# Optimization experiments

Measured on AMD Instinct MI355X. Metric: run time of the kernel, lower is better.

The kernel has to match this reference:

```python
import jax, jax.numpy as jnp
import numpy as np

H = 1024   # hidden_size == memory_size
NH = 4     # num_attention_heads
HD = H // NH
M = 8192   # total memory items
B, S = 4, 2048
EPS = 1e-5


def _ln(x, g, b):
    mu = jnp.mean(x, -1, keepdims=True)
    var = jnp.mean((x - mu) ** 2, -1, keepdims=True)
    return (x - mu) / jnp.sqrt(var + EPS) * g + b


def setup_inputs() -> dict:
    key = jax.random.key(0)
    ks = jax.random.split(key, 16)
    s = 0.02
    return {
        "query_hidden": jax.random.normal(ks[0], (B, S, H), jnp.float32),
        "mem_keys": jax.random.normal(ks[1], (M, H), jnp.float32),
        "importance": jax.random.uniform(ks[2], (M,), jnp.float32),
        "recency": jax.random.uniform(ks[3], (M,), jnp.float32),
        "access_count": jax.random.uniform(ks[4], (M,), jnp.float32),
        "Wq": s * jax.random.normal(ks[5], (H, H), jnp.float32),
        "bq": jnp.zeros((H,), jnp.float32),
        "in_w": s * jax.random.normal(ks[6], (3 * H, H), jnp.float32),
        "in_b": jnp.zeros((3 * H,), jnp.float32),
        "out_w": s * jax.random.normal(ks[7], (H, H), jnp.float32),
        "out_b": jnp.zeros((H,), jnp.float32),
        "gate_w": s * jax.random.normal(ks[8], (H, 2 * H), jnp.float32),
        "gate_b": jnp.zeros((H,), jnp.float32),
        "int_w1": s * jax.random.normal(ks[9], (2 * H, 2 * H), jnp.float32),
        "int_b1": jnp.zeros((2 * H,), jnp.float32),
        "int_ln_g": jnp.ones((2 * H,), jnp.float32),
        "int_ln_b": jnp.zeros((2 * H,), jnp.float32),
        "int_w2": s * jax.random.normal(ks[10], (H, 2 * H), jnp.float32),
        "int_b2": jnp.zeros((H,), jnp.float32),
        "ln1_g": jnp.ones((H,), jnp.float32),
        "ln1_b": jnp.zeros((H,), jnp.float32),
        "ln2_g": jnp.ones((H,), jnp.float32),
        "ln2_b": jnp.zeros((H,), jnp.float32),
        "sel_params": jnp.ones((3,), jnp.float32) / 3.0,
        "top_k": 2048,
    }


def reference(query_hidden, mem_keys, importance, recency, access_count,
              Wq, bq, in_w, in_b, out_w, out_b, gate_w, gate_b,
              int_w1, int_b1, int_ln_g, int_ln_b, int_w2, int_b2,
              ln1_g, ln1_b, ln2_g, ln2_b, sel_params, top_k):
    b, s, _ = query_hidden.shape
    # HTPS selection: softmax-weighted mix of importance / recency / frequency
    w = jax.nn.softmax(sel_params)
    freq = access_count / jnp.max(access_count)
    sel = w[0] * importance + w[1] * recency + w[2] * freq
    _, idx = jax.lax.top_k(sel, top_k)
    mem = mem_keys[idx]                      # [K, H]
    mem_n = _ln(mem, ln1_g, ln1_b)           # layer_norm1 on memory

    q = query_hidden @ Wq.T + bq             # query_proj  [B,S,H]
    wq, wk, wv = in_w[:H], in_w[H:2 * H], in_w[2 * H:]
    bqi, bki, bvi = in_b[:H], in_b[H:2 * H], in_b[2 * H:]
    # Batched MHA: the per-position loop is equivalent to all S queries at once
    Q = (q @ wq.T + bqi).reshape(b, s, NH, HD)
    K = (mem_n @ wk.T + bki).reshape(top_k, NH, HD)   # shared across batch
    V = (mem_n @ wv.T + bvi).reshape(top_k, NH, HD)
    scores = jnp.einsum('bshd,khd->bhsk', Q, K) / jnp.sqrt(jnp.float32(HD))
    attn = jax.nn.softmax(scores, axis=-1)
    ctx = jnp.einsum('bhsk,khd->bshd', attn, V).reshape(b, s, H)
    attn_out = ctx @ out_w.T + out_b

    cat = jnp.concatenate([query_hidden, attn_out], axis=-1)   # [B,S,2H]
    gate = jax.nn.sigmoid(cat @ gate_w.T + gate_b)
    h1 = _ln(cat @ int_w1.T + int_b1, int_ln_g, int_ln_b)
    integ = jax.nn.gelu(h1, approximate=False) @ int_w2.T + int_b2
    return _ln(query_hidden + gate * integ, ln2_g, ln2_b)
```

## Files before the change

### kernel.cpp

```cpp
#include <hip/hip_runtime.h>

#define HDIM 1024
#define MMEM 8192
#define TOPK 2048
#define NROWS 8192
#define LNEPS 1e-5f

typedef unsigned short ushort_t;
typedef __bf16 bf16x8 __attribute__((ext_vector_type(8)));
typedef float f32x4 __attribute__((ext_vector_type(4)));
typedef __attribute__((address_space(1))) const void GVoid;
typedef __attribute__((address_space(3))) void LVoid;

__device__ __forceinline__ ushort_t f2bf(float f) {
    union { float f; unsigned u; } c; c.f = f;
    unsigned r = c.u + 0x7fffu + ((c.u >> 16) & 1u);
    return (ushort_t)(r >> 16);
}
__device__ __forceinline__ float bf2f(ushort_t u) {
    union { unsigned u; float f; } c; c.u = ((unsigned)u) << 16; return c.f;
}
__device__ __forceinline__ float blk_red(float v, int op, float* red) {
    #pragma unroll
    for (int o = 32; o; o >>= 1) {
        float u = __shfl_down(v, o);
        v = op ? fmaxf(v, u) : v + u;
    }
    if ((threadIdx.x & 63) == 0) red[threadIdx.x >> 6] = v;
    __syncthreads();
    float r = op ? fmaxf(fmaxf(red[0], red[1]), fmaxf(red[2], red[3]))
                 : (red[0] + red[1]) + (red[2] + red[3]);
    __syncthreads();
    return r;
}

__global__ __launch_bounds__(256) void sel_prep(const float* __restrict__ sp,
        const float* __restrict__ imp, const float* __restrict__ rec,
        const float* __restrict__ ac, float* __restrict__ sel) {
    __shared__ float red[4];
    float p0 = sp[0], p1 = sp[1], p2 = sp[2];
    float mx = fmaxf(p0, fmaxf(p1, p2));
    float e0 = expf(p0 - mx), e1 = expf(p1 - mx), e2 = expf(p2 - mx);
    float inv = 1.f / (e0 + e1 + e2);
    float w0 = e0 * inv, w1 = e1 * inv, w2 = e2 * inv;
    float m = -1e30f;
    for (int i = threadIdx.x; i < MMEM; i += 256) m = fmaxf(m, ac[i]);
    m = blk_red(m, 1, red);
    float rinv = 1.f / m;
    for (int i = threadIdx.x; i < MMEM; i += 256)
        sel[i] = w0 * imp[i] + w1 * rec[i] + w2 * (ac[i] * rinv);
}

__global__ __launch_bounds__(256) void topk_rank(const float* __restrict__ sel,
                                                 int* __restrict__ idx) {
    __shared__ float s[MMEM];
    __shared__ int pc[256];
    for (int t = threadIdx.x; t < MMEM / 4; t += 256)
        reinterpret_cast<float4*>(s)[t] = reinterpret_cast<const float4*>(sel)[t];
    __syncthreads();
    const int li = threadIdx.x & 31;
    const int jc = threadIdx.x >> 5;
    const int i  = blockIdx.x * 32 + li;
    const float si = s[i];
    int cnt = 0;
    const float4* sv = reinterpret_cast<const float4*>(s) + jc * 256;
    #pragma unroll 4
    for (int t = 0; t < 256; ++t) {
        float4 v = sv[t];
        int j0 = jc * 1024 + t * 4;
        cnt += (v.x > si) || (v.x == si && (j0 + 0) < i);
        cnt += (v.y > si) || (v.y == si && (j0 + 1) < i);
        cnt += (v.z > si) || (v.z == si && (j0 + 2) < i);
        cnt += (v.w > si) || (v.w == si && (j0 + 3) < i);
    }
    pc[threadIdx.x] = cnt;
    __syncthreads();
    if (threadIdx.x < 32) {
        int r = 0;
        #pragma unroll
        for (int c = 0; c < 8; ++c) r += pc[c * 32 + threadIdx.x];
        if (r < TOPK) idx[r] = blockIdx.x * 32 + threadIdx.x;
    }
}

__global__ __launch_bounds__(256) void gather_ln(const float* __restrict__ mem_keys,
        const int* __restrict__ idx, const float* __restrict__ g,
        const float* __restrict__ b, ushort_t* __restrict__ out) {
    __shared__ float red[4];
    int src = idx[blockIdx.x] & (MMEM - 1);
    const float* x = mem_keys + (size_t)src * HDIM;
    float4 v = reinterpret_cast<const float4*>(x)[threadIdx.x];
    float s = v.x + v.y + v.z + v.w;
    float ss = v.x*v.x + v.y*v.y + v.z*v.z + v.w*v.w;
    s  = blk_red(s, 0, red);
    ss = blk_red(ss, 0, red);
    float mu = s * (1.f / HDIM);
    float var = ss * (1.f / HDIM) - mu * mu;
    float rstd = rsqrtf(var + LNEPS);
    int c = threadIdx.x * 4;
    ushort4 o;
    o.x = f2bf((v.x - mu) * rstd * g[c+0] + b[c+0]);
    o.y = f2bf((v.y - mu) * rstd * g[c+1] + b[c+1]);
    o.z = f2bf((v.z - mu) * rstd * g[c+2] + b[c+2]);
    o.w = f2bf((v.w - mu) * rstd * g[c+3] + b[c+3]);
    *reinterpret_cast<ushort4*>(out + (size_t)blockIdx.x * HDIM + c) = o;
}

__global__ __launch_bounds__(256) void cvt_all(const float* __restrict__ in_w,
        const float* __restrict__ out_w, const float* __restrict__ gate_w,
        const float* __restrict__ int_w1, const float* __restrict__ int_w2,
        ushort_t* __restrict__ inw_bf, ushort_t* __restrict__ outw_bf,
        ushort_t* __restrict__ gw3, ushort_t* __restrict__ intw2_bf) {
    const int b = blockIdx.x;
    const float* src; ushort_t* dst; int rel;
    if      (b < 3072)  { src = in_w;   dst = inw_bf;        rel = b; }
    else if (b < 4096)  { src = out_w;  dst = outw_bf;       rel = b - 3072; }
    else if (b < 6144)  { src = gate_w; dst = gw3;           rel = b - 4096; }
    else if (b < 10240) { src = int_w1; dst = gw3 + 2097152; rel = b - 6144; }
    else                { src = int_w2; dst = intw2_bf;      rel = b - 10240; }
    size_t i = ((size_t)rel * 256 + threadIdx.x) * 4;
    float4 v = *reinterpret_cast<const float4*>(src + i);
    ushort4 o = { f2bf(v.x), f2bf(v.y), f2bf(v.z), f2bf(v.w) };
    *reinterpret_cast<ushort4*>(dst + i) = o;
}

__global__ __launch_bounds__(256) void cvt_t_bf16(const float* __restrict__ in,
                                                  ushort_t* __restrict__ out) {
    __shared__ ushort_t t[64][65];
    const int bx = blockIdx.x * 64, by = blockIdx.y * 64;
    const int r = threadIdx.x >> 4, c4 = (threadIdx.x & 15) << 2;
    #pragma unroll
    for (int rr = 0; rr < 64; rr += 16) {
        float4 v = *reinterpret_cast<const float4*>(in + (size_t)(by + r + rr) * 1024 + bx + c4);
        t[r + rr][c4 + 0] = f2bf(v.x);
        t[r + rr][c4 + 1] = f2bf(v.y);
        t[r + rr][c4 + 2] = f2bf(v.z);
        t[r + rr][c4 + 3] = f2bf(v.w);
    }
    __syncthreads();
    #pragma unroll
    for (int rr = 0; rr < 64; rr += 16) {
        const int i = r + rr;
        ushort4 o = { t[c4 + 0][i], t[c4 + 1][i], t[c4 + 2][i], t[c4 + 3][i] };
        *reinterpret_cast<ushort4*>(out + (size_t)(bx + i) * 1024 + by + c4) = o;
    }
}

__global__ __launch_bounds__(256) void bias_fold(const float* __restrict__ wq,
        const float* __restrict__ bq, const float* __restrict__ bqi,
        float* __restrict__ beff) {
    __shared__ float red[4];
    const float4 wv = reinterpret_cast<const float4*>(wq + (size_t)blockIdx.x * 1024)[threadIdx.x];
    const float4 bv = reinterpret_cast<const float4*>(bq)[threadIdx.x];
    float s = wv.x*bv.x + wv.y*bv.y + wv.z*bv.z + wv.w*bv.w;
    s = blk_red(s, 0, red);
    if (threadIdx.x == 0) beff[blockIdx.x] = s + bqi[blockIdx.x];
}

__global__ __launch_bounds__(256) void cvt_x_cat(const float* __restrict__ x,
                                                 ushort_t* __restrict__ cat) {
    size_t i = ((size_t)blockIdx.x * 256 + threadIdx.x) * 4;
    size_t row = i >> 10, col = i & 1023;
    float4 v = *reinterpret_cast<const float4*>(x + i);
    ushort4 o = { f2bf(v.x), f2bf(v.y), f2bf(v.z), f2bf(v.w) };
    *reinterpret_cast<ushort4*>(cat + row * 2048 + col) = o;
}

__global__ __launch_bounds__(256) void softmax_rows(ushort_t* __restrict__ sc) {
    const int row = blockIdx.x * 4 + (threadIdx.x >> 6);
    const int l = threadIdx.x & 63;
    uint4* p = reinterpret_cast<uint4*>(sc + (size_t)row * 2048 + l * 32);
    uint4 u[4];
    #pragma unroll
    for (int i = 0; i < 4; ++i) u[i] = p[i];
    float v[32];
    #pragma unroll
    for (int i = 0; i < 4; ++i) {
        unsigned* w = reinterpret_cast<unsigned*>(&u[i]);
        #pragma unroll
        for (int k = 0; k < 4; ++k) {
            union { unsigned u; float f; } lo, hi;
            lo.u = w[k] << 16; hi.u = w[k] & 0xffff0000u;
            v[i*8 + k*2]     = lo.f;
            v[i*8 + k*2 + 1] = hi.f;
        }
    }
    float mx = v[0];
    #pragma unroll
    for (int j = 1; j < 32; ++j) mx = fmaxf(mx, v[j]);
    #pragma unroll
    for (int o = 1; o < 64; o <<= 1) mx = fmaxf(mx, __shfl_xor(mx, o));
    float s = 0.f;
    #pragma unroll
    for (int j = 0; j < 32; ++j) { v[j] = expf(v[j] - mx); s += v[j]; }
    #pragma unroll
    for (int o = 1; o < 64; o <<= 1) s += __shfl_xor(s, o);
    float inv = 1.f / s;
    #pragma unroll
    for (int i = 0; i < 4; ++i) {
        unsigned* w = reinterpret_cast<unsigned*>(&u[i]);
        #pragma unroll
        for (int k = 0; k < 4; ++k) {
            unsigned lo = f2bf(v[i*8 + k*2] * inv);
            unsigned hi = f2bf(v[i*8 + k*2 + 1] * inv);
            w[k] = lo | (hi << 16);
        }
    }
    #pragma unroll
    for (int i = 0; i < 4; ++i) p[i] = u[i];
}

__global__ __launch_bounds__(256) void ln_gelu(ushort_t* h1,
        const float* __restrict__ g, const float* __restrict__ b) {
    __shared__ float red[4];
    ushort_t* p = h1 + (size_t)blockIdx.x * 2048 + threadIdx.x * 8;
    ushort4 a = reinterpret_cast<const ushort4*>(p)[0];
    ushort4 c = reinterpret_cast<const ushort4*>(p)[1];
    float v[8] = { bf2f(a.x), bf2f(a.y), bf2f(a.z), bf2f(a.w),
                   bf2f(c.x), bf2f(c.y), bf2f(c.z), bf2f(c.w) };
    float s = 0.f, ss = 0.f;
    #pragma unroll
    for (int j = 0; j < 8; ++j) { s += v[j]; ss += v[j]*v[j]; }
    s  = blk_red(s, 0, red);
    ss = blk_red(ss, 0, red);
    float mu = s * (1.f / 2048.f);
    float var = ss * (1.f / 2048.f) - mu * mu;
    float rstd = rsqrtf(var + LNEPS);
    int c0 = threadIdx.x * 8;
    ushort_t o[8];
    #pragma unroll
    for (int j = 0; j < 8; ++j) {
        float xn = (v[j] - mu) * rstd * g[c0 + j] + b[c0 + j];
        float ge = 0.5f * xn * (1.f + erff(xn * 0.70710678118654752f));
        o[j] = f2bf(ge);
    }
    ushort4 o1 = { o[0], o[1], o[2], o[3] };
    ushort4 o2 = { o[4], o[5], o[6], o[7] };
    reinterpret_cast<ushort4*>(p)[0] = o1;
    reinterpret_cast<ushort4*>(p)[1] = o2;
}

__global__ __launch_bounds__(256) void final_ln(const float* __restrict__ x,
        const ushort_t* __restrict__ gate, const ushort_t* __restrict__ integ,
        const float* __restrict__ g, const float* __restrict__ b,
        float* __restrict__ out) {
    __shared__ float red[4];
    size_t base = (size_t)blockIdx.x * HDIM + threadIdx.x * 4;
    float4 xv = *reinterpret_cast<const float4*>(x + base);
    ushort4 gv = *reinterpret_cast<const ushort4*>(gate + base);
    ushort4 iv = *reinterpret_cast<const ushort4*>(integ + base);
    float v[4] = { xv.x + bf2f(gv.x)*bf2f(iv.x), xv.y + bf2f(gv.y)*bf2f(iv.y),
                   xv.z + bf2f(gv.z)*bf2f(iv.z), xv.w + bf2f(gv.w)*bf2f(iv.w) };
    float s = v[0]+v[1]+v[2]+v[3];
    float ss = v[0]*v[0]+v[1]*v[1]+v[2]*v[2]+v[3]*v[3];
    s  = blk_red(s, 0, red);
    ss = blk_red(ss, 0, red);
    float mu = s * (1.f / HDIM);
    float var = ss * (1.f / HDIM) - mu * mu;
    float rstd = rsqrtf(var + LNEPS);
    int c = threadIdx.x * 4;
    float4 o;
    o.x = (v[0] - mu) * rstd * g[c+0] + b[c+0];
    o.y = (v[1] - mu) * rstd * g[c+1] + b[c+1];
    o.z = (v[2] - mu) * rstd * g[c+2] + b[c+2];
    o.w = (v[3] - mu) * rstd * g[c+3] + b[c+3];
    *reinterpret_cast<float4*>(out + base) = o;
}

template<int EPI, int BIAS>
__global__ __launch_bounds__(256, 2)
void gemm_bt(const ushort_t* __restrict__ A, const ushort_t* __restrict__ B,
             const float* __restrict__ bias, void* __restrict__ Cv,
             void* __restrict__ Cv2, const float* __restrict__ bias2,
             int K, int lda, int ldb, int ldc,
             long long sA1, long long sA2, long long sAz,
             long long sB1, long long sB2, long long sBz,
             long long sC1, long long sC2, long long sCz,
             int z2n, int zbase, float scale)
{
    __shared__ __align__(16) ushort_t As[8192];
    __shared__ __align__(16) ushort_t Bs[8192];
    const int zz = blockIdx.z;
    const int zg = zz + zbase;
    const int z1 = zg / z2n, z2 = zg - z1 * z2n;
    A += (size_t)(z1 * sA1 + z2 * sA2 + zz * sAz);
    B += (size_t)(z1 * sB1 + z2 * sB2 + zz * sBz);
    const size_t cOff = (size_t)(z1 * sC1 + z2 * sC2 + zz * sCz);

    const int nwg = gridDim.x * gridDim.y;
    const int wg  = blockIdx.y * gridDim.x + blockIdx.x;
    const int q8  = nwg >> 3, r8 = nwg & 7;
    const int xcd = wg & 7, lo = wg >> 3;
    const int wgid = (xcd < r8 ? xcd * (q8 + 1) : r8 * (q8 + 1) + (xcd - r8) * q8) + lo;
    const int m0 = (wgid / gridDim.x) * 128, n0 = (wgid % gridDim.x) * 128;

    const int tid = threadIdx.x;
    const int w = tid >> 6, l = tid & 63;
    const int wm = w >> 1, wn = w & 1;

    f32x4 acc[4][4] = {};
    const int srow = l >> 3;
    const int scol = ((l & 7) ^ srow) << 3;

    for (int k0 = 0; k0 < K; k0 += 64) {
        #pragma unroll
        for (int i = 0; i < 4; ++i) {
            const int c = i * 4 + w;
            const int row = c * 8 + srow;
            const ushort_t* ga = A + (size_t)(m0 + row) * lda + (k0 + scol);
            const ushort_t* gb = B + (size_t)(n0 + row) * ldb + (k0 + scol);
            __builtin_amdgcn_global_load_lds((GVoid*)ga, (LVoid*)(As + c * 512), 16, 0, 0);
            __builtin_amdgcn_global_load_lds((GVoid*)gb, (LVoid*)(Bs + c * 512), 16, 0, 0);
        }
        __syncthreads();
        #pragma unroll
        for (int kk = 0; kk < 2; ++kk) {
            bf16x8 af[4], bfv[4];
            #pragma unroll
            for (int m = 0; m < 4; ++m) {
                const int row = wm * 64 + m * 16 + (l & 15);
                const int cb = ((kk * 64) + ((l >> 4) * 16)) ^ ((row & 7) << 4);
                af[m] = *reinterpret_cast<const bf16x8*>(
                    reinterpret_cast<const char*>(As) + row * 128 + cb);
            }
            #pragma unroll
            for (int n = 0; n < 4; ++n) {
                const int row = wn * 64 + n * 16 + (l & 15);
                const int cb = ((kk * 64) + ((l >> 4) * 16)) ^ ((row & 7) << 4);
                bfv[n] = *reinterpret_cast<const bf16x8*>(
                    reinterpret_cast<const char*>(Bs) + row * 128 + cb);
            }
            #pragma unroll
            for (int m = 0; m < 4; ++m)
                #pragma unroll
                for (int n = 0; n < 4; ++n)
                    acc[m][n] = __builtin_amdgcn_mfma_f32_16x16x32_bf16(
                        af[m], bfv[n], acc[m][n], 0, 0, 0);
        }
        __syncthreads();
    }

    #pragma unroll
    for (int m = 0; m < 4; ++m) {
        const int grow = m0 + wm * 64 + m * 16 + ((l >> 4) << 2);
        #pragma unroll
        for (int n = 0; n < 4; ++n) {
            const int gcol = n0 + wn * 64 + n * 16 + (l & 15);
            float bc = (BIAS == 1) ? bias[gcol] : 0.f;
            #pragma unroll
            for (int j = 0; j < 4; ++j) {
                if (EPI == 3) {
                    float v = acc[m][n][j];
                    if (gcol < 1024) {
                        v += bias[gcol];
                        v = 1.f / (1.f + expf(-v));
                        ((ushort_t*)Cv)[(size_t)(grow + j) * ldc + gcol] = f2bf(v);
                    } else {
                        v += bias2[gcol - 1024];
                        ((ushort_t*)Cv2)[(size_t)(grow + j) * 2048 + (gcol - 1024)] = f2bf(v);
                    }
                } else {
                    float v = acc[m][n][j] * scale;
                    if (BIAS == 1) v += bc;
                    if (BIAS == 2) v += bias[grow + j];
                    if (EPI == 2) v = 1.f / (1.f + expf(-v));
                    const size_t off = cOff + (size_t)(grow + j) * ldc + gcol;
                    if (EPI == 1) ((ushort_t*)Cv)[off] = f2bf(v);
                    else          ((float*)Cv)[off]    = v;
                }
            }
        }
    }
}

extern "C" void kernel_launch(void* const* d_in, const int* in_sizes, int n_in,
                              void* d_out, int out_size, void* d_ws, size_t ws_size,
                              hipStream_t stream) {
    const float* x          = (const float*)d_in[0];
    const float* mem_keys   = (const float*)d_in[1];
    const float* importance = (const float*)d_in[2];
    const float* recency    = (const float*)d_in[3];
    const float* access_cnt = (const float*)d_in[4];
    const float* Wq         = (const float*)d_in[5];
    const float* bq         = (const float*)d_in[6];
    const float* in_w       = (const float*)d_in[7];
    const float* in_b       = (const float*)d_in[8];
    const float* out_w      = (const float*)d_in[9];
    const float* out_b      = (const float*)d_in[10];
    const float* gate_w     = (const float*)d_in[11];
    const float* gate_b     = (const float*)d_in[12];
    const float* int_w1     = (const float*)d_in[13];
    const float* int_b1     = (const float*)d_in[14];
    const float* int_ln_g   = (const float*)d_in[15];
    const float* int_ln_b   = (const float*)d_in[16];
    const float* int_w2     = (const float*)d_in[17];
    const float* int_b2     = (const float*)d_in[18];
    const float* ln1_g      = (const float*)d_in[19];
    const float* ln1_b      = (const float*)d_in[20];
    const float* ln2_g      = (const float*)d_in[21];
    const float* ln2_b      = (const float*)d_in[22];
    const float* sel_params = (const float*)d_in[23];

    char* ws = (char*)d_ws;
    size_t off = 0;
    auto alloc = [&](size_t bytes) -> char* {
        char* p = ws + off;
        off = (off + bytes + 255) & ~(size_t)255;
        return p;
    };

    float*    sel      = (float*)alloc(MMEM * 4);
    int*      idx      = (int*)alloc(TOPK * 4);
    float*    beff     = (float*)alloc(1024 * 4);
    ushort_t* wqT_bf   = (ushort_t*)alloc((size_t)1048576 * 2);
    ushort_t* weff_bf  = (ushort_t*)alloc((size_t)1048576 * 2);
    ushort_t* inw_bf   = (ushort_t*)alloc((size_t)3145728 * 2);
    ushort_t* outw_bf  = (ushort_t*)alloc((size_t)1048576 * 2);
    ushort_t* gw3      = (ushort_t*)alloc((size_t)6291456 * 2);
    ushort_t* intw2_bf = (ushort_t*)alloc((size_t)2097152 * 2);
    ushort_t* mem_n    = (ushort_t*)alloc((size_t)TOPK * HDIM * 2);
    ushort_t* Kbuf     = (ushort_t*)alloc((size_t)TOPK * HDIM * 2);
    ushort_t* Vt       = (ushort_t*)alloc((size_t)HDIM * TOPK * 2);
    ushort_t* cat      = (ushort_t*)alloc((size_t)NROWS * 2048 * 2);
    ushort_t* qQ       = (ushort_t*)alloc((size_t)NROWS * 2048 * 2);
    ushort_t* Qbuf     = qQ + (size_t)NROWS * HDIM;
    ushort_t* h1       = qQ;
    ushort_t* ctx      = (ushort_t*)alloc((size_t)NROWS * HDIM * 2);
    ushort_t* integ    = ctx;

    int NC = 16;
    while (NC > 1 && off + (size_t)NC * 8388608 > ws_size) NC >>= 1;
    ushort_t* scores = (ushort_t*)alloc((size_t)NC * 8388608);
    ushort_t* gatev  = scores;

    cvt_t_bf16<<<dim3(16,16), 256, 0, stream>>>(Wq, wqT_bf);
    cvt_all<<<12288, 256, 0, stream>>>(in_w, out_w, gate_w, int_w1, int_w2,
                                       inw_bf, outw_bf, gw3, intw2_bf);
    cvt_x_cat<<<8192, 256, 0, stream>>>(x, cat);
    bias_fold<<<1024, 256, 0, stream>>>(in_w, bq, in_b, beff);

    gemm_bt<1,0><<<dim3(8,8,1), 256, 0, stream>>>(inw_bf, wqT_bf, nullptr, weff_bf,
        nullptr, nullptr, 1024, 1024, 1024, 1024, 0,0,0, 0,0,0, 0,0,0, 1, 0, 1.f);

    sel_prep<<<1, 256, 0, stream>>>(sel_params, importance, recency, access_cnt, sel);
    topk_rank<<<MMEM/32, 256, 0, stream>>>(sel, idx);
    gather_ln<<<TOPK, 256, 0, stream>>>(mem_keys, idx, ln1_g, ln1_b, mem_n);

    gemm_bt<1,1><<<dim3(8,64,1), 256, 0, stream>>>(cat, weff_bf, beff, Qbuf,
        nullptr, nullptr, 1024, 2048, 1024, 1024, 0,0,0, 0,0,0, 0,0,0, 1, 0, 1.f);
    gemm_bt<1,1><<<dim3(8,16,1), 256, 0, stream>>>(mem_n, inw_bf + 1048576, in_b + 1024,
        Kbuf, nullptr, nullptr, 1024, 1024, 1024, 1024, 0,0,0, 0,0,0, 0,0,0, 1, 0, 1.f);
    gemm_bt<1,2><<<dim3(16,8,1), 256, 0, stream>>>(inw_bf + 2097152, mem_n, in_b + 2048,
        Vt, nullptr, nullptr, 1024, 1024, 1024, 2048, 0,0,0, 0,0,0, 0,0,0, 1, 0, 1.f);

    for (int c0 = 0; c0 < 16; c0 += NC) {
        gemm_bt<1,0><<<dim3(16,16,NC), 256, 0, stream>>>(Qbuf, Kbuf, nullptr, scores,
            nullptr, nullptr, 256, 1024, 1024, 2048,
            2097152, 256, 0,  0, 256, 0,  0, 0, 4194304, 4, c0, 0.0625f);
        softmax_rows<<<NC * 512, 256, 0, stream>>>(scores);
        gemm_bt<1,0><<<dim3(2,16,NC), 256, 0, stream>>>(scores, Vt, nullptr, ctx,
            nullptr, nullptr, 2048, 2048, 2048, 1024,
            0, 0, 4194304,  0, 524288, 0,  2097152, 256, 0, 4, c0, 1.f);
    }

    gemm_bt<1,1><<<dim3(8,64,1), 256, 0, stream>>>(ctx, outw_bf, out_b,
        (void*)(cat + 1024), nullptr, nullptr, 1024, 1024, 1024, 2048,
        0,0,0, 0,0,0, 0,0,0, 1, 0, 1.f);

    gemm_bt<3,0><<<dim3(24,64,1), 256, 0, stream>>>(cat, gw3, gate_b, gatev,
        h1, int_b1, 2048, 2048, 2048, 1024, 0,0,0, 0,0,0, 0,0,0, 1, 0, 1.f);

    ln_gelu<<<NROWS, 256, 0, stream>>>(h1, int_ln_g, int_ln_b);
    gemm_bt<1,1><<<dim3(8,64,1), 256, 0, stream>>>(h1, intw2_bf, int_b2, integ,
        nullptr, nullptr, 2048, 2048, 2048, 1024, 0,0,0, 0,0,0, 0,0,0, 1, 0, 1.f);
    final_ln<<<NROWS, 256, 0, stream>>>(x, gatev, integ, ln2_g, ln2_b, (float*)d_out);
}
```

Measured before the change: 584.1 us.

## Fold out_proj into gate/int_w1 weights and split-K over x and ctx

Removes the separate out_proj GEMM by precomputing folded weights (the attn_out half of gate_w/int_w1 multiplied by out_w) and folded biases. The gate/int GEMM then reads x and ctx directly through a two-source split-K path instead of a materialized concat buffer, which saves an 8192x1024x1024 GEMM and the cat writes. The cost is a small weight-fold GEMM, an extra transpose-convert of out_w, and bias-fold kernels per call. It also swaps expf for __expf in the softmax and sigmoid epilogues, which slightly changes precision.

```diff
diff --git a/kernel.cpp b/kernel.cpp
--- a/kernel.cpp
+++ b/kernel.cpp
@@ -106,18 +106,25 @@
     *reinterpret_cast<ushort4*>(out + (size_t)blockIdx.x * HDIM + c) = o;
 }
 
+__global__ __launch_bounds__(256) void cvt_bf16(const float* __restrict__ in,
+                                                ushort_t* __restrict__ out) {
+    size_t i = ((size_t)blockIdx.x * 256 + threadIdx.x) * 4;
+    float4 v = *reinterpret_cast<const float4*>(in + i);
+    ushort4 o = { f2bf(v.x), f2bf(v.y), f2bf(v.z), f2bf(v.w) };
+    *reinterpret_cast<ushort4*>(out + i) = o;
+}
+
 __global__ __launch_bounds__(256) void cvt_all(const float* __restrict__ in_w,
-        const float* __restrict__ out_w, const float* __restrict__ gate_w,
-        const float* __restrict__ int_w1, const float* __restrict__ int_w2,
-        ushort_t* __restrict__ inw_bf, ushort_t* __restrict__ outw_bf,
-        ushort_t* __restrict__ gw3, ushort_t* __restrict__ intw2_bf) {
+        const float* __restrict__ gate_w, const float* __restrict__ int_w1,
+        const float* __restrict__ int_w2,
+        ushort_t* __restrict__ inw_bf, ushort_t* __restrict__ gw3,
+        ushort_t* __restrict__ intw2_bf) {
     const int b = blockIdx.x;
     const float* src; ushort_t* dst; int rel;
-    if      (b < 3072)  { src = in_w;   dst = inw_bf;        rel = b; }
-    else if (b < 4096)  { src = out_w;  dst = outw_bf;       rel = b - 3072; }
-    else if (b < 6144)  { src = gate_w; dst = gw3;           rel = b - 4096; }
-    else if (b < 10240) { src = int_w1; dst = gw3 + 2097152; rel = b - 6144; }
-    else                { src = int_w2; dst = intw2_bf;      rel = b - 10240; }
+    if      (b < 3072) { src = in_w;   dst = inw_bf;        rel = b; }
+    else if (b < 5120) { src = gate_w; dst = gw3;           rel = b - 3072; }
+    else if (b < 9216) { src = int_w1; dst = gw3 + 2097152; rel = b - 5120; }
+    else               { src = int_w2; dst = intw2_bf;      rel = b - 9216; }
     size_t i = ((size_t)rel * 256 + threadIdx.x) * 4;
     float4 v = *reinterpret_cast<const float4*>(src + i);
     ushort4 o = { f2bf(v.x), f2bf(v.y), f2bf(v.z), f2bf(v.w) };
@@ -157,13 +164,20 @@
     if (threadIdx.x == 0) beff[blockIdx.x] = s + bqi[blockIdx.x];
 }
 
-__global__ __launch_bounds__(256) void cvt_x_cat(const float* __restrict__ x,
-                                                 ushort_t* __restrict__ cat) {
-    size_t i = ((size_t)blockIdx.x * 256 + threadIdx.x) * 4;
-    size_t row = i >> 10, col = i & 1023;
-    float4 v = *reinterpret_cast<const float4*>(x + i);
-    ushort4 o = { f2bf(v.x), f2bf(v.y), f2bf(v.z), f2bf(v.w) };
-    *reinterpret_cast<ushort4*>(cat + row * 2048 + col) = o;
+__global__ __launch_bounds__(256) void bias_fold3(const float* __restrict__ gate_w,
+        const float* __restrict__ int_w1, const float* __restrict__ gate_b,
+        const float* __restrict__ int_b1, const float* __restrict__ out_b,
+        float* __restrict__ beff3) {
+    __shared__ float red[4];
+    const int j = blockIdx.x;
+    const float* wrow = (j < 1024 ? gate_w + (size_t)j * 2048
+                                  : int_w1 + (size_t)(j - 1024) * 2048) + 1024;
+    const float4 wv = reinterpret_cast<const float4*>(wrow)[threadIdx.x];
+    const float4 bv = reinterpret_cast<const float4*>(out_b)[threadIdx.x];
+    float s = wv.x*bv.x + wv.y*bv.y + wv.z*bv.z + wv.w*bv.w;
+    s = blk_red(s, 0, red);
+    if (threadIdx.x == 0)
+        beff3[j] = s + (j < 1024 ? gate_b[j] : int_b1[j - 1024]);
 }
 
 __global__ __launch_bounds__(256) void softmax_rows(ushort_t* __restrict__ sc) {
@@ -192,7 +206,7 @@
     for (int o = 1; o < 64; o <<= 1) mx = fmaxf(mx, __shfl_xor(mx, o));
     float s = 0.f;
     #pragma unroll
-    for (int j = 0; j < 32; ++j) { v[j] = expf(v[j] - mx); s += v[j]; }
+    for (int j = 0; j < 32; ++j) { v[j] = __expf(v[j] - mx); s += v[j]; }
     #pragma unroll
     for (int o = 1; o < 64; o <<= 1) s += __shfl_xor(s, o);
     float inv = 1.f / s;
@@ -267,15 +281,17 @@
     *reinterpret_cast<float4*>(out + base) = o;
 }
 
-template<int EPI, int BIAS>
+template<int EPI, int BIAS, int SPLIT>
 __global__ __launch_bounds__(256, 2)
 void gemm_bt(const ushort_t* __restrict__ A, const ushort_t* __restrict__ B,
+             const ushort_t* __restrict__ A2, const ushort_t* __restrict__ B2,
+             int lda2, int ldb2,
              const float* __restrict__ bias, void* __restrict__ Cv,
              void* __restrict__ Cv2, const float* __restrict__ bias2,
              int K, int lda, int ldb, int ldc,
-             long long sA1, long long sA2, long long sAz,
-             long long sB1, long long sB2, long long sBz,
-             long long sC1, long long sC2, long long sCz,
+             long long sA1, long long sA2s, long long sAz,
+             long long sB1, long long sB2s, long long sBz,
+             long long sC1, long long sC2s, long long sCz,
              int z2n, int zbase, float scale)
 {
     __shared__ __align__(16) ushort_t As[8192];
@@ -283,9 +299,9 @@
     const int zz = blockIdx.z;
     const int zg = zz + zbase;
     const int z1 = zg / z2n, z2 = zg - z1 * z2n;
-    A += (size_t)(z1 * sA1 + z2 * sA2 + zz * sAz);
-    B += (size_t)(z1 * sB1 + z2 * sB2 + zz * sBz);
-    const size_t cOff = (size_t)(z1 * sC1 + z2 * sC2 + zz * sCz);
+    A += (size_t)(z1 * sA1 + z2 * sA2s + zz * sAz);
+    B += (size_t)(z1 * sB1 + z2 * sB2s + zz * sBz);
+    const size_t cOff = (size_t)(z1 * sC1 + z2 * sC2s + zz * sCz);
 
     const int nwg = gridDim.x * gridDim.y;
     const int wg  = blockIdx.y * gridDim.x + blockIdx.x;
@@ -303,12 +319,15 @@
     const int scol = ((l & 7) ^ srow) << 3;
 
     for (int k0 = 0; k0 < K; k0 += 64) {
+        const ushort_t* Ab = A; const ushort_t* Bb = B;
+        int la = lda, lb = ldb, kk0 = k0;
+        if (SPLIT && k0 >= 1024) { Ab = A2; Bb = B2; la = lda2; lb = ldb2; kk0 = k0 - 1024; }
         #pragma unroll
         for (int i = 0; i < 4; ++i) {
             const int c = i * 4 + w;
             const int row = c * 8 + srow;
-            const ushort_t* ga = A + (size_t)(m0 + row) * lda + (k0 + scol);
-            const ushort_t* gb = B + (size_t)(n0 + row) * ldb + (k0 + scol);
+            const ushort_t* ga = Ab + (size_t)(m0 + row) * la + (kk0 + scol);
+            const ushort_t* gb = Bb + (size_t)(n0 + row) * lb + (kk0 + scol);
             __builtin_amdgcn_global_load_lds((GVoid*)ga, (LVoid*)(As + c * 512), 16, 0, 0);
             __builtin_amdgcn_global_load_lds((GVoid*)gb, (LVoid*)(Bs + c * 512), 16, 0, 0);
         }
@@ -353,7 +372,7 @@
                     float v = acc[m][n][j];
                     if (gcol < 1024) {
                         v += bias[gcol];
-                        v = 1.f / (1.f + expf(-v));
+                        v = 1.f / (1.f + __expf(-v));
                         ((ushort_t*)Cv)[(size_t)(grow + j) * ldc + gcol] = f2bf(v);
                     } else {
                         v += bias2[gcol - 1024];
@@ -363,7 +382,7 @@
                     float v = acc[m][n][j] * scale;
                     if (BIAS == 1) v += bc;
                     if (BIAS == 2) v += bias[grow + j];
-                    if (EPI == 2) v = 1.f / (1.f + expf(-v));
+                    if (EPI == 2) v = 1.f / (1.f + __expf(-v));
                     const size_t off = cOff + (size_t)(grow + j) * ldc + gcol;
                     if (EPI == 1) ((ushort_t*)Cv)[off] = f2bf(v);
                     else          ((float*)Cv)[off]    = v;
@@ -412,16 +431,18 @@
     float*    sel      = (float*)alloc(MMEM * 4);
     int*      idx      = (int*)alloc(TOPK * 4);
     float*    beff     = (float*)alloc(1024 * 4);
+    float*    beff3    = (float*)alloc(3072 * 4);
     ushort_t* wqT_bf   = (ushort_t*)alloc((size_t)1048576 * 2);
+    ushort_t* outwT_bf = (ushort_t*)alloc((size_t)1048576 * 2);
     ushort_t* weff_bf  = (ushort_t*)alloc((size_t)1048576 * 2);
     ushort_t* inw_bf   = (ushort_t*)alloc((size_t)3145728 * 2);
-    ushort_t* outw_bf  = (ushort_t*)alloc((size_t)1048576 * 2);
     ushort_t* gw3      = (ushort_t*)alloc((size_t)6291456 * 2);
+    ushort_t* wfold3   = (ushort_t*)alloc((size_t)3145728 * 2);
     ushort_t* intw2_bf = (ushort_t*)alloc((size_t)2097152 * 2);
     ushort_t* mem_n    = (ushort_t*)alloc((size_t)TOPK * HDIM * 2);
     ushort_t* Kbuf     = (ushort_t*)alloc((size_t)TOPK * HDIM * 2);
     ushort_t* Vt       = (ushort_t*)alloc((size_t)HDIM * TOPK * 2);
-    ushort_t* cat      = (ushort_t*)alloc((size_t)NROWS * 2048 * 2);
+    ushort_t* xbf      = (ushort_t*)alloc((size_t)NROWS * HDIM * 2);
     ushort_t* qQ       = (ushort_t*)alloc((size_t)NROWS * 2048 * 2);
     ushort_t* Qbuf     = qQ + (size_t)NROWS * HDIM;
     ushort_t* h1       = qQ;
@@ -434,44 +455,53 @@
     ushort_t* gatev  = scores;
 
     cvt_t_bf16<<<dim3(16,16), 256, 0, stream>>>(Wq, wqT_bf);
-    cvt_all<<<12288, 256, 0, stream>>>(in_w, out_w, gate_w, int_w1, int_w2,
-                                       inw_bf, outw_bf, gw3, intw2_bf);
-    cvt_x_cat<<<8192, 256, 0, stream>>>(x, cat);
+    cvt_t_bf16<<<dim3(16,16), 256, 0, stream>>>(out_w, outwT_bf);
+    cvt_all<<<11264, 256, 0, stream>>>(in_w, gate_w, int_w1, int_w2,
+                                       inw_bf, gw3, intw2_bf);
+    cvt_bf16<<<8192, 256, 0, stream>>>(x, xbf);
     bias_fold<<<1024, 256, 0, stream>>>(in_w, bq, in_b, beff);
-
-    gemm_bt<1,0><<<dim3(8,8,1), 256, 0, stream>>>(inw_bf, wqT_bf, nullptr, weff_bf,
-        nullptr, nullptr, 1024, 1024, 1024, 1024, 0,0,0, 0,0,0, 0,0,0, 1, 0, 1.f);
+    bias_fold3<<<3072, 256, 0, stream>>>(gate_w, int_w1, gate_b, int_b1, out_b, beff3);
+
+    gemm_bt<1,0,0><<<dim3(8,8,1), 256, 0, stream>>>(inw_bf, wqT_bf,
+        nullptr, nullptr, 0, 0, nullptr, weff_bf, nullptr, nullptr,
+        1024, 1024, 1024, 1024, 0,0,0, 0,0,0, 0,0,0, 1, 0, 1.f);
+    gemm_bt<1,0,0><<<dim3(8,24,1), 256, 0, stream>>>(gw3 + 1024, outwT_bf,
+        nullptr, nullptr, 0, 0, nullptr, wfold3, nullptr, nullptr,
+        1024, 2048, 1024, 1024, 0,0,0, 0,0,0, 0,0,0, 1, 0, 1.f);
 
     sel_prep<<<1, 256, 0, stream>>>(sel_params, importance, recency, access_cnt, sel);
     topk_rank<<<MMEM/32, 256, 0, stream>>>(sel, idx);
     gather_ln<<<TOPK, 256, 0, stream>>>(mem_keys, idx, ln1_g, ln1_b, mem_n);
 
-    gemm_bt<1,1><<<dim3(8,64,1), 256, 0, stream>>>(cat, weff_bf, beff, Qbuf,
-        nullptr, nullptr, 1024, 2048, 1024, 1024, 0,0,0, 0,0,0, 0,0,0, 1, 0, 1.f);
-    gemm_bt<1,1><<<dim3(8,16,1), 256, 0, stream>>>(mem_n, inw_bf + 1048576, in_b + 1024,
-        Kbuf, nullptr, nullptr, 1024, 1024, 1024, 1024, 0,0,0, 0,0,0, 0,0,0, 1, 0, 1.f);
-    gemm_bt<1,2><<<dim3(16,8,1), 256, 0, stream>>>(inw_bf + 2097152, mem_n, in_b + 2048,
-        Vt, nullptr, nullptr, 1024, 1024, 1024, 2048, 0,0,0, 0,0,0, 0,0,0, 1, 0, 1.f);
+    gemm_bt<1,1,0><<<dim3(8,64,1), 256, 0, stream>>>(xbf, weff_bf,
+        nullptr, nullptr, 0, 0, beff, Qbuf, nullptr, nullptr,
+        1024, 1024, 1024, 1024, 0,0,0, 0,0,0, 0,0,0, 1, 0, 1.f);
+    gemm_bt<1,1,0><<<dim3(8,16,1), 256, 0, stream>>>(mem_n, inw_bf + 1048576,
+        nullptr, nullptr, 0, 0, in_b + 1024, Kbuf, nullptr, nullptr,
+        1024, 1024, 1024, 1024, 0,0,0, 0,0,0, 0,0,0, 1, 0, 1.f);
+    gemm_bt<1,2,0><<<dim3(16,8,1), 256, 0, stream>>>(inw_bf + 2097152, mem_n,
+        nullptr, nullptr, 0, 0, in_b + 2048, Vt, nullptr, nullptr,
+        1024, 1024, 1024, 2048, 0,0,0, 0,0,0, 0,0,0, 1, 0, 1.f);
 
     for (int c0 = 0; c0 < 16; c0 += NC) {
-        gemm_bt<1,0><<<dim3(16,16,NC), 256, 0, stream>>>(Qbuf, Kbuf, nullptr, scores,
-            nullptr, nullptr, 256, 1024, 1024, 2048,
+        gemm_bt<1,0,0><<<dim3(16,16,NC), 256, 0, stream>>>(Qbuf, Kbuf,
+            nullptr, nullptr, 0, 0, nullptr, scores, nullptr, nullptr,
+            256, 1024, 1024, 2048,
             2097152, 256, 0,  0, 256, 0,  0, 0, 4194304, 4, c0, 0.0625f);
         softmax_rows<<<NC * 512, 256, 0, stream>>>(scores);
-        gemm_bt<1,0><<<dim3(2,16,NC), 256, 0, stream>>>(scores, Vt, nullptr, ctx,
-            nullptr, nullptr, 2048, 2048, 2048, 1024,
+        gemm_bt<1,0,0><<<dim3(2,16,NC), 256, 0, stream>>>(scores, Vt,
+            nullptr, nullptr, 0, 0, nullptr, ctx, nullptr, nullptr,
+            2048, 2048, 2048, 1024,
             0, 0, 4194304,  0, 524288, 0,  2097152, 256, 0, 4, c0, 1.f);
     }
 
-    gemm_bt<1,1><<<dim3(8,64,1), 256, 0, stream>>>(ctx, outw_bf, out_b,
-        (void*)(cat + 1024), nullptr, nullptr, 1024, 1024, 1024, 2048,
-        0,0,0, 0,0,0, 0,0,0, 1, 0, 1.f);
-
-    gemm_bt<3,0><<<dim3(24,64,1), 256, 0, stream>>>(cat, gw3, gate_b, gatev,
-        h1, int_b1, 2048, 2048, 2048, 1024, 0,0,0, 0,0,0, 0,0,0, 1, 0, 1.f);
+    gemm_bt<3,0,1><<<dim3(24,64,1), 256, 0, stream>>>(xbf, gw3,
+        ctx, wfold3, 1024, 1024, beff3, gatev, h1, beff3 + 1024,
+        2048, 1024, 2048, 1024, 0,0,0, 0,0,0, 0,0,0, 1, 0, 1.f);
 
     ln_gelu<<<NROWS, 256, 0, stream>>>(h1, int_ln_g, int_ln_b);
-    gemm_bt<1,1><<<dim3(8,64,1), 256, 0, stream>>>(h1, intw2_bf, int_b2, integ,
-        nullptr, nullptr, 2048, 2048, 2048, 1024, 0,0,0, 0,0,0, 0,0,0, 1, 0, 1.f);
+    gemm_bt<1,1,0><<<dim3(8,64,1), 256, 0, stream>>>(h1, intw2_bf,
+        nullptr, nullptr, 0, 0, int_b2, integ, nullptr, nullptr,
+        2048, 2048, 2048, 1024, 0,0,0, 0,0,0, 0,0,0, 1, 0, 1.f);
     final_ln<<<NROWS, 256, 0, stream>>>(x, gatev, integ, ln2_g, ln2_b, (float*)d_out);
 }
```

Result: faster. 572.5 us (-2.0%).
